# Kernel optimization log

Measured on AMD Instinct MI355X. Metric: run time of the kernel, lower is better.

## Reference

```python
import jax, jax.numpy as jnp
import numpy as np

# model config (see init_kwargs)
L, H, NH, KVH, DH, I, P, F, T = 8, 1024, 16, 2, 64, 4096, 4, 64, 10
QLEN = 9                      # 1 dit token + P cond tokens + P latent tokens
GROUPS = NH // KVH            # GQA repeat factor
PREFIX = P + 1                # prefix_plus
SCALE = DH ** -0.25           # folded into rope cos/sin (applied to q AND k)


def setup_inputs() -> dict:
    key = jax.random.key(0)
    ks = jax.random.split(key, 16)
    g = lambda i, shape, s=0.02: jax.random.normal(ks[i], shape, jnp.float32) * s
    # sway-sampled timestep schedule -> dt table (matches torch precompute)
    ts = np.linspace(1.0, 0.0, T + 1, dtype=np.float32)
    ts = (ts + 1.0 * (np.cos(np.pi / 2 * ts) - 1.0 + ts))[1:]
    dt_all = jnp.asarray((ts[:-1] - ts[1:]).reshape(1, 1, T - 1))
    # rope tables with attention scale folded in
    pos = np.arange(QLEN, dtype=np.float32)
    inv_freq = 1.0 / (10000.0 ** (np.arange(0, DH, 2, dtype=np.float32) / DH))
    freqs = np.concatenate([np.outer(pos, inv_freq)] * 2, axis=-1)  # [QLEN, DH]
    cos_q = jnp.asarray(np.cos(freqs)[None, None] * SCALE)  # [1,1,QLEN,DH]
    sin_q = jnp.asarray(np.sin(freqs)[None, None] * SCALE)
    return dict(
        random=g(0, (1, P, F), 1.0),
        dit_hidden=g(1, (1, 1, H), 1.0),
        feat_cond=g(2, (2, P, H), 1.0),
        cfg_value=jnp.full((1,), 2.5, jnp.float32),
        cfg_value_minus=jnp.full((1,), -1.5, jnp.float32),
        t_all=g(3, (1, T - 1, H), 1.0),   # precomputed time_mlp output table
        dt_all=dt_all, cos_q=cos_q, sin_q=sin_q,
        W_in=g(4, (F, H)), b_in=jnp.zeros((H,), jnp.float32),
        ln1_w=jnp.ones((L, H), jnp.float32),
        Wq=g(5, (L, H, NH * DH)), Wk=g(6, (L, H, KVH * DH)),
        Wv=g(7, (L, H, KVH * DH)), Wo=g(8, (L, NH * DH, H)),
        ln2_w=jnp.ones((L, H), jnp.float32),
        Wg=g(9, (L, H, I)), Wu=g(10, (L, H, I)), Wd=g(11, (L, I, H)),
        norm_w=jnp.ones((H,), jnp.float32),
        W_out=g(12, (H, F)), b_out=jnp.zeros((F,), jnp.float32),
        step=jnp.zeros((1,), jnp.int32),
    )


def _rms(x, w, eps=1e-6):
    return x * jax.lax.rsqrt(jnp.mean(x * x, axis=-1, keepdims=True) + eps) * w


def _rot_half(x):
    x1, x2 = jnp.split(x, 2, axis=-1)
    return jnp.concatenate([-x2, x1], axis=-1)


def reference(random, dit_hidden, feat_cond, cfg_value, cfg_value_minus,
              t_all, dt_all, cos_q, sin_q, W_in, b_in, ln1_w, Wq, Wk, Wv, Wo,
              ln2_w, Wg, Wu, Wd, norm_w, W_out, b_out, step):
    t = t_all[:, step]                                   # [1,1,H]
    dt = dt_all[..., step]                               # [1,1,1]
    dh = jnp.concatenate([dit_hidden + t, t], axis=0)    # CFG doubling -> [2,1,H]
    x = random @ W_in + b_in                             # [1,P,H]
    h = jnp.concatenate([dh, feat_cond, jnp.concatenate([x, x], axis=0)], axis=1)  # [2,QLEN,H]

    def layer(h, p):
        ln1, wq, wk, wv, wo, ln2, wg, wu, wd = p
        hn = _rms(h, ln1)
        q = (hn @ wq).reshape(2, QLEN, NH, DH).transpose(0, 2, 1, 3)
        k = (hn @ wk).reshape(2, QLEN, KVH, DH).transpose(0, 2, 1, 3)
        v = (hn @ wv).reshape(2, QLEN, KVH, DH).transpose(0, 2, 1, 3)
        # rope with head_dim**-0.25 scale folded into cos/sin (applied to q and k)
        q = q * cos_q + _rot_half(q) * sin_q
        k = k * cos_q + _rot_half(k) * sin_q
        k = jnp.repeat(k, GROUPS, axis=1)                # repeat_k (GQA)
        v = jnp.repeat(v, GROUPS, axis=1)                # repeat_v
        attn = jax.nn.softmax(jnp.einsum('bhqd,bhkd->bhqk', q, k), axis=-1)
        out = jnp.einsum('bhqk,bhkd->bhqd', attn, v)
        out = out.transpose(0, 2, 1, 3).reshape(2, QLEN, NH * DH)
        h = h + out @ wo
        hn2 = _rms(h, ln2)
        h = h + (jax.nn.silu(hn2 @ wg) * (hn2 @ wu)) @ wd
        return h, None

    h, _ = jax.lax.scan(layer, h, (ln1_w, Wq, Wk, Wv, Wo, ln2_w, Wg, Wu, Wd))
    h = _rms(h[:, PREFIX:], norm_w)                      # drop prefix -> [2,P,H]
    out = h @ W_out + b_out                              # [2,P,F]
    pos, neg = out[0:1], out[1:2]
    pf = pos.reshape(1, 1, -1)                           # [1,1,P*F]
    nf = neg.reshape(1, -1, 1)                           # [1,P*F,1]
    st = (pf @ nf) / (jnp.swapaxes(nf, 1, 2) @ nf + 1e-7)  # rescaled CFG, [1,1,1]
    dphi = cfg_value_minus * neg * st + cfg_value * pos
    next_random = random - dt * dphi
    return step + 1, next_random
```

## Files before the change

### kernel.cpp

```cpp
#include <hip/hip_runtime.h>

#define TOKENS 18
#define QLEN 9
#define HDIM 1024
#define IDIM 4096
#define NLAYER 8

#define H_OFF     0u
#define QKV_OFF   18432u
#define QKVP_OFF  41472u
#define OPP_OFF   2990592u
#define WDP_OFF   7709184u
#define GUP_OFF   12427776u
#define OUTP_OFF  17146368u
#define TOTAL_F   17162752u

__device__ __forceinline__ void load8(float4* buf, const float* wp, int cc, int stride) {
#pragma unroll
  for (int j = 0; j < 8; j++)
    buf[j] = *reinterpret_cast<const float4*>(wp + (size_t)(cc * 8 + j) * stride);
}
__device__ __forceinline__ void fma8(float4* acc, const float4* buf,
                                     const float (*sb)[TOKENS], int cc) {
#pragma unroll
  for (int j = 0; j < 8; j++) {
#pragma unroll
    for (int t = 0; t < TOKENS; t++) {
      float bv = sb[cc * 8 + j][t];
      acc[t].x += bv * buf[j].x; acc[t].y += bv * buf[j].y;
      acc[t].z += bv * buf[j].z; acc[t].w += bv * buf[j].w;
    }
  }
}

__device__ __forceinline__ void block_rstd18(const float* __restrict__ h,
                                             float* s_rstd, float* s_red) {
  int tid = threadIdx.x;
  float ss[TOKENS];
#pragma unroll
  for (int t = 0; t < TOKENS; t++) {
    float4 v = reinterpret_cast<const float4*>(h + (size_t)t * HDIM)[tid];
    ss[t] = v.x*v.x + v.y*v.y + v.z*v.z + v.w*v.w;
  }
#pragma unroll
  for (int off = 32; off >= 1; off >>= 1) {
#pragma unroll
    for (int t = 0; t < TOKENS; t++) ss[t] += __shfl_down(ss[t], off);
  }
  int wave = tid >> 6, lane = tid & 63;
  if (lane == 0) {
#pragma unroll
    for (int t = 0; t < TOKENS; t++) s_red[wave * TOKENS + t] = ss[t];
  }
  __syncthreads();
  if (tid < TOKENS) {
    float tot = s_red[tid] + s_red[TOKENS + tid] + s_red[2*TOKENS + tid] + s_red[3*TOKENS + tid];
    s_rstd[tid] = rsqrtf(tot * (1.0f / HDIM) + 1e-6f);
  }
  __syncthreads();
}

__global__ __launch_bounds__(256) void k_red4(
    const float* __restrict__ src, float* __restrict__ dst,
    int nparts, int n, int accum) {
  int le = threadIdx.x & 63, j = threadIdx.x >> 6;
  int e = blockIdx.x * 64 + le;
  float s = 0.f;
#pragma unroll 8
  for (int p = j; p < nparts; p += 4) s += src[(size_t)p * n + e];
  __shared__ float red[4][64];
  red[j][le] = s;
  __syncthreads();
  if (j == 0) {
    float tot = red[0][le] + red[1][le] + red[2][le] + red[3][le];
    dst[e] = accum ? dst[e] + tot : tot;
  }
}

__global__ __launch_bounds__(256) void k_embed(
    const float* __restrict__ rnd, const float* __restrict__ dit,
    const float* __restrict__ feat, const float* __restrict__ t_all,
    const float* __restrict__ W_in, const float* __restrict__ b_in,
    const int* __restrict__ step, float* __restrict__ ws) {
  float* h = ws;
  int bid = blockIdx.x, tid = threadIdx.x;
  int st = step[0];
  const float* t = t_all + (size_t)st * HDIM;
  if (bid < 2) {
    int b = bid;
    for (int c = tid; c < HDIM; c += 256) {
      float v = t[c];
      if (b == 0) v += dit[c];
      h[(size_t)(b * QLEN) * HDIM + c] = v;
    }
  } else if (bid < 10) {
    int i = bid - 2;
    int b = i >> 2, p = i & 3;
    for (int c = tid; c < HDIM; c += 256)
      h[(size_t)(b * QLEN + 1 + p) * HDIM + c] = feat[(size_t)(b * 4 + p) * HDIM + c];
  } else {
    int p = bid - 10;
    __shared__ float rl[64];
    if (tid < 64) rl[tid] = rnd[p * 64 + tid];
    __syncthreads();
    for (int c = tid; c < HDIM; c += 256) {
      float acc = b_in[c];
#pragma unroll 8
      for (int f = 0; f < 64; f++) acc += rl[f] * W_in[(size_t)f * HDIM + c];
      h[(size_t)(5 + p) * HDIM + c] = acc;
      h[(size_t)(QLEN + 5 + p) * HDIM + c] = acc;
    }
  }
}

__global__ __launch_bounds__(256) void k_qkv(
    const float* __restrict__ Wq, const float* __restrict__ Wk,
    const float* __restrict__ Wv, const float* __restrict__ ln1,
    float* __restrict__ ws, int layer) {
  const float* h = ws;
  __shared__ float s_rstd[TOKENS];
  __shared__ float s_red[4 * TOKENS];
  __shared__ float s_b[8][TOKENS];
  int tid = threadIdx.x;
  block_rstd18(h, s_rstd, s_red);
  int r0 = blockIdx.y * 8;
  const float* lw = ln1 + (size_t)layer * HDIM;
  for (int i = tid; i < 8 * TOKENS; i += 256) {
    int r = i / TOKENS, t = i - r * TOKENS;
    s_b[r][t] = h[(size_t)t * HDIM + r0 + r] * lw[r0 + r];
  }
  __syncthreads();
  float* qpb = ws + QKVP_OFF + (size_t)blockIdx.y * (TOKENS * 1280);
  if (blockIdx.x == 0) {
    int c = tid * 4;
    const float* wp = Wq + ((size_t)layer << 20) + (size_t)r0 * HDIM + c;
    float4 A[8];
    load8(A, wp, 0, HDIM);
    float4 acc[TOKENS];
#pragma unroll
    for (int t = 0; t < TOKENS; t++) acc[t] = make_float4(0.f, 0.f, 0.f, 0.f);
    fma8(acc, A, s_b, 0);
#pragma unroll
    for (int t = 0; t < TOKENS; t++) {
      float rs = s_rstd[t];
      float4 o = make_float4(acc[t].x*rs, acc[t].y*rs, acc[t].z*rs, acc[t].w*rs);
      *reinterpret_cast<float4*>(qpb + (size_t)t * 1280 + c) = o;
    }
  } else if (tid < 64) {
    int c = 1024 + tid * 4;
    const float* wp;
    if (c < 1152) wp = Wk + (size_t)layer * 131072 + (size_t)r0 * 128 + (c - 1024);
    else          wp = Wv + (size_t)layer * 131072 + (size_t)r0 * 128 + (c - 1152);
    float4 A[8];
    load8(A, wp, 0, 128);
    float4 acc[TOKENS];
#pragma unroll
    for (int t = 0; t < TOKENS; t++) acc[t] = make_float4(0.f, 0.f, 0.f, 0.f);
    fma8(acc, A, s_b, 0);
#pragma unroll
    for (int t = 0; t < TOKENS; t++) {
      float rs = s_rstd[t];
      float4 o = make_float4(acc[t].x*rs, acc[t].y*rs, acc[t].z*rs, acc[t].w*rs);
      *reinterpret_cast<float4*>(qpb + (size_t)t * 1280 + c) = o;
    }
  }
}

__global__ __launch_bounds__(256) void k_attn(
    const float* __restrict__ Wo, const float* __restrict__ cosq,
    const float* __restrict__ sinq, float* __restrict__ ws, int layer) {
  const float* qkv = ws + QKV_OFF;
  int by = blockIdx.x;
  float* op = ws + OPP_OFF + (size_t)by * (TOKENS * HDIM);
  __shared__ float lq[2][QLEN][68];
  __shared__ float lk[2][QLEN][68];
  __shared__ float lv[2][QLEN][4];
  __shared__ float sP[2][QLEN][12];
  __shared__ float sA[4][TOKENS];
  int tid = threadIdx.x;
  int r0 = by * 4;
  int head = r0 >> 6;
  int kvh = head >> 3;
  int d0 = r0 & 63;
  for (int i = tid; i < 2 * QLEN * 64; i += 256) {
    int d = i & 63;
    int qi = (i >> 6) % QLEN;
    int b = i / (QLEN * 64);
    const float* qr = qkv + (size_t)(b * QLEN + qi) * 1280;
    float c = cosq[qi * 64 + d], s = sinq[qi * 64 + d];
    float qv = qr[head * 64 + d];
    float qo = (d < 32) ? -qr[head * 64 + d + 32] : qr[head * 64 + d - 32];
    lq[b][qi][d] = qv * c + qo * s;
    float kv = qr[1024 + kvh * 64 + d];
    float ko = (d < 32) ? -qr[1024 + kvh * 64 + d + 32] : qr[1024 + kvh * 64 + d - 32];
    lk[b][qi][d] = kv * c + ko * s;
  }
  for (int i = tid; i < 2 * QLEN * 4; i += 256) {
    int d = i & 3;
    int ki = (i >> 2) % QLEN;
    int b = i / (QLEN * 4);
    lv[b][ki][d] = qkv[(size_t)(b * QLEN + ki) * 1280 + 1152 + kvh * 64 + d0 + d];
  }
  __syncthreads();
  for (int i = tid; i < 2 * QLEN * QLEN; i += 256) {
    int ki = i % QLEN;
    int qi = (i / QLEN) % QLEN;
    int b = i / (QLEN * QLEN);
    float s = 0.f;
#pragma unroll
    for (int d = 0; d < 64; d++) s += lq[b][qi][d] * lk[b][ki][d];
    sP[b][qi][ki] = s;
  }
  __syncthreads();
  if (tid < TOKENS) {
    int b = tid / QLEN, qi = tid % QLEN;
    float m = -1e30f;
#pragma unroll
    for (int k = 0; k < QLEN; k++) m = fmaxf(m, sP[b][qi][k]);
    float e[QLEN], sum = 0.f;
#pragma unroll
    for (int k = 0; k < QLEN; k++) { e[k] = expf(sP[b][qi][k] - m); sum += e[k]; }
    float inv = 1.f / sum;
#pragma unroll
    for (int k = 0; k < QLEN; k++) sP[b][qi][k] = e[k] * inv;
  }
  __syncthreads();
  for (int i = tid; i < 4 * TOKENS; i += 256) {
    int dd = i / TOKENS, t = i - dd * TOKENS;
    int b = t / QLEN, qi = t % QLEN;
    float a = 0.f;
#pragma unroll
    for (int k = 0; k < QLEN; k++) a += sP[b][qi][k] * lv[b][k][dd];
    sA[dd][t] = a;
  }
  __syncthreads();
  int c = tid * 4;
  const float* wp = Wo + ((size_t)layer << 20) + (size_t)r0 * HDIM + c;
  float4 wv[4];
#pragma unroll
  for (int r = 0; r < 4; r++)
    wv[r] = *reinterpret_cast<const float4*>(wp + (size_t)r * HDIM);
  float4 acc[TOKENS];
#pragma unroll
  for (int t = 0; t < TOKENS; t++) acc[t] = make_float4(0.f, 0.f, 0.f, 0.f);
#pragma unroll
  for (int r = 0; r < 4; r++) {
#pragma unroll
    for (int t = 0; t < TOKENS; t++) {
      float bv = sA[r][t];
      acc[t].x += bv * wv[r].x; acc[t].y += bv * wv[r].y;
      acc[t].z += bv * wv[r].z; acc[t].w += bv * wv[r].w;
    }
  }
#pragma unroll
  for (int t = 0; t < TOKENS; t++)
    *reinterpret_cast<float4*>(op + (size_t)t * HDIM + c) = acc[t];
}

__global__ __launch_bounds__(256) void k_gu(
    const float* __restrict__ Wg, const float* __restrict__ Wu,
    const float* __restrict__ ln2, float* __restrict__ ws, int layer) {
  const float* h = ws;
  __shared__ float s_rstd[TOKENS];
  __shared__ float s_red[4 * TOKENS];
  __shared__ float s_b[32][TOKENS];
  int tid = threadIdx.x;
  block_rstd18(h, s_rstd, s_red);
  int cg = blockIdx.x, ks = blockIdx.y, r0 = ks * 32;
  const float* lw = ln2 + (size_t)layer * HDIM;
  for (int i = tid; i < 32 * TOKENS; i += 256) {
    int r = i / TOKENS, t = i - r * TOKENS;
    s_b[r][t] = h[(size_t)t * HDIM + r0 + r] * lw[r0 + r];
  }
  __syncthreads();
  const float* W = (cg < 4 ? Wg : Wu) + ((size_t)layer << 22);
  int c = (cg & 3) * 1024 + tid * 4;
  const float* wp = W + (size_t)r0 * IDIM + c;
  float4 A[8], B[8];
  float4 acc[TOKENS];
#pragma unroll
  for (int t = 0; t < TOKENS; t++) acc[t] = make_float4(0.f, 0.f, 0.f, 0.f);
  load8(A, wp, 0, IDIM);
  load8(B, wp, 1, IDIM);
  fma8(acc, A, s_b, 0);
  load8(A, wp, 2, IDIM);
  fma8(acc, B, s_b, 1);
  load8(B, wp, 3, IDIM);
  fma8(acc, A, s_b, 2);
  fma8(acc, B, s_b, 3);
  float* gp = ws + GUP_OFF + (size_t)ks * (TOKENS * 8192) + cg * 1024 + tid * 4;
#pragma unroll
  for (int t = 0; t < TOKENS; t++) {
    float rs = s_rstd[t];
    float4 o = make_float4(acc[t].x*rs, acc[t].y*rs, acc[t].z*rs, acc[t].w*rs);
    *reinterpret_cast<float4*>(gp + (size_t)t * 8192) = o;
  }
}

__global__ __launch_bounds__(256) void k_wd(
    const float* __restrict__ Wd, float* __restrict__ ws, int layer) {
  const float* gup = ws + GUP_OFF;
  int by = blockIdx.x;
  int r0 = by * 16;
  __shared__ float s_b[16][TOKENS];
  int tid = threadIdx.x;
  for (int i = tid; i < 16 * TOKENS; i += 256) {
    int r = i / TOKENS, t = i - r * TOKENS;
    const float* base = gup + (size_t)t * 8192 + r0 + r;
    float g = 0.f, u = 0.f;
#pragma unroll 8
    for (int p = 0; p < 32; p++) {
      g += base[(size_t)p * (TOKENS * 8192)];
      u += base[(size_t)p * (TOKENS * 8192) + 4096];
    }
    s_b[r][t] = (g / (1.f + expf(-g))) * u;
  }
  __syncthreads();
  int c = tid * 4;
  const float* wp = Wd + ((size_t)layer << 22) + (size_t)r0 * HDIM + c;
  float4 A[8], B[8];
  float4 acc[TOKENS];
#pragma unroll
  for (int t = 0; t < TOKENS; t++) acc[t] = make_float4(0.f, 0.f, 0.f, 0.f);
  load8(A, wp, 0, HDIM);
  load8(B, wp, 1, HDIM);
  fma8(acc, A, s_b, 0);
  fma8(acc, B, s_b, 1);
  float* wdp = ws + WDP_OFF + (size_t)by * (TOKENS * HDIM);
#pragma unroll
  for (int t = 0; t < TOKENS; t++)
    *reinterpret_cast<float4*>(wdp + (size_t)t * HDIM + c) = acc[t];
}

__global__ __launch_bounds__(256) void k_out(
    const float* __restrict__ Wout, const float* __restrict__ normw,
    float* __restrict__ ws) {
  const float* h = ws;
  float* outp = ws + OUTP_OFF;
  __shared__ float s_rstd[8];
  __shared__ float s_red[32];
  __shared__ float s_b[128][8];
  int tid = threadIdx.x;
  float ss[8];
#pragma unroll
  for (int s = 0; s < 8; s++) {
    int tix = (s >> 2) * QLEN + 5 + (s & 3);
    float4 v = reinterpret_cast<const float4*>(h + (size_t)tix * HDIM)[tid];
    ss[s] = v.x*v.x + v.y*v.y + v.z*v.z + v.w*v.w;
  }
#pragma unroll
  for (int off = 32; off >= 1; off >>= 1) {
#pragma unroll
    for (int s = 0; s < 8; s++) ss[s] += __shfl_down(ss[s], off);
  }
  int wave = tid >> 6, lane = tid & 63;
  if (lane == 0) {
#pragma unroll
    for (int s = 0; s < 8; s++) s_red[wave * 8 + s] = ss[s];
  }
  __syncthreads();
  if (tid < 8) {
    float tot = s_red[tid] + s_red[8 + tid] + s_red[16 + tid] + s_red[24 + tid];
    s_rstd[tid] = rsqrtf(tot * (1.f / HDIM) + 1e-6f);
  }
  __syncthreads();
  int r0 = blockIdx.x * 128;
  for (int i = tid; i < 128 * 8; i += 256) {
    int r = i >> 3, s = i & 7;
    int tix = (s >> 2) * QLEN + 5 + (s & 3);
    s_b[r][s] = h[(size_t)tix * HDIM + r0 + r] * normw[r0 + r] * s_rstd[s];
  }
  __syncthreads();
  int colc = tid & 63, rsub = tid >> 6;
  const float* wp = Wout + (size_t)(r0 + rsub * 32) * 64 + colc;
  float acc[8];
#pragma unroll
  for (int s = 0; s < 8; s++) acc[s] = 0.f;
#pragma unroll 8
  for (int r = 0; r < 32; r++) {
    float w = wp[(size_t)r * 64];
#pragma unroll
    for (int s = 0; s < 8; s++) acc[s] += s_b[rsub * 32 + r][s] * w;
  }
  float* slot = outp + (size_t)(blockIdx.x * 4 + rsub) * 512;
#pragma unroll
  for (int s = 0; s < 8; s++) slot[s * 64 + colc] = acc[s];
}

__global__ __launch_bounds__(256) void k_final(
    const float* __restrict__ rnd, const float* __restrict__ cfg,
    const float* __restrict__ cfgm, const float* __restrict__ dt_all,
    const float* __restrict__ bout, const int* __restrict__ step,
    const float* __restrict__ ws, float* __restrict__ out) {
  const float* outp = ws + OUTP_OFF;
  int tid = threadIdx.x;
  int f = tid & 63;
  float p = bout[f], n = bout[f];
#pragma unroll 8
  for (int pp = 0; pp < 32; pp++) {
    p += outp[(size_t)pp * 512 + tid];
    n += outp[(size_t)pp * 512 + 256 + tid];
  }
  float pn = p * n, nn = n * n;
#pragma unroll
  for (int off = 32; off >= 1; off >>= 1) {
    pn += __shfl_down(pn, off);
    nn += __shfl_down(nn, off);
  }
  __shared__ float red[8];
  __shared__ float s_st;
  int wave = tid >> 6, lane = tid & 63;
  if (lane == 0) { red[wave] = pn; red[4 + wave] = nn; }
  __syncthreads();
  if (tid == 0) {
    float PN = red[0] + red[1] + red[2] + red[3];
    float NN = red[4] + red[5] + red[6] + red[7];
    s_st = PN / (NN + 1e-7f);
  }
  __syncthreads();
  int st = step[0];
  float dphi = cfgm[0] * n * s_st + cfg[0] * p;
  float next = rnd[tid] - dt_all[st] * dphi;
  if (tid == 0) out[0] = (float)(st + 1);
  out[1 + tid] = next;
}

extern "C" void kernel_launch(void* const* d_in, const int* in_sizes, int n_in,
                              void* d_out, int out_size, void* d_ws, size_t ws_size,
                              hipStream_t stream) {
  const float* rnd   = (const float*)d_in[0];
  const float* dit   = (const float*)d_in[1];
  const float* feat  = (const float*)d_in[2];
  const float* cfg   = (const float*)d_in[3];
  const float* cfgm  = (const float*)d_in[4];
  const float* t_all = (const float*)d_in[5];
  const float* dt_al = (const float*)d_in[6];
  const float* cosq  = (const float*)d_in[7];
  const float* sinq  = (const float*)d_in[8];
  const float* W_in  = (const float*)d_in[9];
  const float* b_in  = (const float*)d_in[10];
  const float* ln1   = (const float*)d_in[11];
  const float* Wq    = (const float*)d_in[12];
  const float* Wk    = (const float*)d_in[13];
  const float* Wv    = (const float*)d_in[14];
  const float* Wo    = (const float*)d_in[15];
  const float* ln2   = (const float*)d_in[16];
  const float* Wg    = (const float*)d_in[17];
  const float* Wu    = (const float*)d_in[18];
  const float* Wd    = (const float*)d_in[19];
  const float* normw = (const float*)d_in[20];
  const float* Wout  = (const float*)d_in[21];
  const float* bout  = (const float*)d_in[22];
  const int*   step  = (const int*)d_in[23];
  float* ws = (float*)d_ws;

  k_embed<<<14, 256, 0, stream>>>(rnd, dit, feat, t_all, W_in, b_in, step, ws);
  for (int l = 0; l < NLAYER; l++) {
    k_qkv<<<dim3(2, 128), 256, 0, stream>>>(Wq, Wk, Wv, ln1, ws, l);
    k_red4<<<360, 256, 0, stream>>>(ws + QKVP_OFF, ws + QKV_OFF, 128, TOKENS * 1280, 0);
    k_attn<<<256, 256, 0, stream>>>(Wo, cosq, sinq, ws, l);
    k_red4<<<288, 256, 0, stream>>>(ws + OPP_OFF, ws + H_OFF, 256, TOKENS * HDIM, 1);
    k_gu<<<dim3(8, 32), 256, 0, stream>>>(Wg, Wu, ln2, ws, l);
    k_wd<<<256, 256, 0, stream>>>(Wd, ws, l);
    k_red4<<<288, 256, 0, stream>>>(ws + WDP_OFF, ws + H_OFF, 256, TOKENS * HDIM, 1);
  }
  k_out<<<8, 256, 0, stream>>>(Wout, normw, ws);
  k_final<<<1, 256, 0, stream>>>(rnd, cfg, cfgm, dt_al, bout, step, ws, (float*)d_out);
}
```

Baseline: 620.6 us.

## Fuse split-K reductions and RMS statistics into neighboring layer kernels

Removes the standalone partial-sum reduction kernels. The attention-output and MLP-down reductions are folded into the gate/up and residual-update kernels, and the residual stream is double-buffered. Per-token sum-of-squares partials are produced wherever the hidden state is written, so each matmul kernel no longer recomputes the RMS norm over the full hidden state. The split-K partitioning is retiled for QKV, Wo and gate/up. An atomic counter with a spin-wait is added so one set of blocks can publish the post-attention rstd to the others. This trades fewer launches and less redundant traffic for redundant partial-sum reads in many blocks and a cross-block dependency that could stall if blocks are not co-resident.

```diff
diff --git a/kernel.cpp b/kernel.cpp
--- a/kernel.cpp
+++ b/kernel.cpp
@@ -6,14 +6,18 @@
 #define IDIM 4096
 #define NLAYER 8
 
-#define H_OFF     0u
-#define QKV_OFF   18432u
-#define QKVP_OFF  41472u
-#define OPP_OFF   2990592u
-#define WDP_OFF   7709184u
-#define GUP_OFF   12427776u
-#define OUTP_OFF  17146368u
-#define TOTAL_F   17162752u
+#define HA_OFF    0u
+#define HB_OFF    18432u
+#define SQP_OFF   36864u
+#define RSTD_OFF  37008u
+#define CNT_OFF   37152u
+#define QKVR_OFF  37248u
+#define QKVP_OFF  60288u
+#define OPP_OFF   797568u
+#define GUP_OFF   1387392u
+#define WDP_OFF   10824576u
+#define OUTP_OFF  15543168u
+#define TOTAL_F   15559552u
 
 __device__ __forceinline__ void load8(float4* buf, const float* wp, int cc, int stride) {
 #pragma unroll
@@ -32,48 +36,32 @@
     }
   }
 }
-
-__device__ __forceinline__ void block_rstd18(const float* __restrict__ h,
-                                             float* s_rstd, float* s_red) {
-  int tid = threadIdx.x;
-  float ss[TOKENS];
-#pragma unroll
-  for (int t = 0; t < TOKENS; t++) {
-    float4 v = reinterpret_cast<const float4*>(h + (size_t)t * HDIM)[tid];
-    ss[t] = v.x*v.x + v.y*v.y + v.z*v.z + v.w*v.w;
-  }
-#pragma unroll
-  for (int off = 32; off >= 1; off >>= 1) {
-#pragma unroll
-    for (int t = 0; t < TOKENS; t++) ss[t] += __shfl_down(ss[t], off);
-  }
-  int wave = tid >> 6, lane = tid & 63;
-  if (lane == 0) {
-#pragma unroll
-    for (int t = 0; t < TOKENS; t++) s_red[wave * TOKENS + t] = ss[t];
-  }
-  __syncthreads();
-  if (tid < TOKENS) {
-    float tot = s_red[tid] + s_red[TOKENS + tid] + s_red[2*TOKENS + tid] + s_red[3*TOKENS + tid];
-    s_rstd[tid] = rsqrtf(tot * (1.0f / HDIM) + 1e-6f);
-  }
-  __syncthreads();
-}
-
-__global__ __launch_bounds__(256) void k_red4(
-    const float* __restrict__ src, float* __restrict__ dst,
-    int nparts, int n, int accum) {
-  int le = threadIdx.x & 63, j = threadIdx.x >> 6;
-  int e = blockIdx.x * 64 + le;
-  float s = 0.f;
-#pragma unroll 8
-  for (int p = j; p < nparts; p += 4) s += src[(size_t)p * n + e];
-  __shared__ float red[4][64];
-  red[j][le] = s;
-  __syncthreads();
-  if (j == 0) {
-    float tot = red[0][le] + red[1][le] + red[2][le] + red[3][le];
-    dst[e] = accum ? dst[e] + tot : tot;
+__device__ __forceinline__ void loadf2(float2* buf, const float* wp, int base, int stride) {
+#pragma unroll
+  for (int j = 0; j < 8; j++)
+    buf[j] = *reinterpret_cast<const float2*>(wp + (size_t)(base + j) * stride);
+}
+__device__ __forceinline__ void fmaf2(float2* acc, const float2* buf,
+                                      const float (*sb)[TOKENS], int base) {
+#pragma unroll
+  for (int j = 0; j < 8; j++) {
+#pragma unroll
+    for (int t = 0; t < TOKENS; t++) {
+      float bv = sb[base + j][t];
+      acc[t].x += bv * buf[j].x; acc[t].y += bv * buf[j].y;
+    }
+  }
+}
+__device__ __forceinline__ void loadf1(float* buf, const float* wp, int base, int stride) {
+#pragma unroll
+  for (int j = 0; j < 8; j++) buf[j] = wp[(size_t)(base + j) * stride];
+}
+__device__ __forceinline__ void fmaf1(float* acc, const float* buf,
+                                      const float (*sb)[TOKENS], int base) {
+#pragma unroll
+  for (int j = 0; j < 8; j++) {
+#pragma unroll
+    for (int t = 0; t < TOKENS; t++) acc[t] += sb[base + j][t] * buf[j];
   }
 }
 
@@ -82,110 +70,118 @@
     const float* __restrict__ feat, const float* __restrict__ t_all,
     const float* __restrict__ W_in, const float* __restrict__ b_in,
     const int* __restrict__ step, float* __restrict__ ws) {
-  float* h = ws;
-  int bid = blockIdx.x, tid = threadIdx.x;
+  int t = blockIdx.x >> 3, ch = blockIdx.x & 7, c0 = ch * 128;
+  int b = t / QLEN, q = t - b * QLEN;
+  int tid = threadIdx.x;
+  __shared__ float hv[128];
+  __shared__ float red[2][128];
+  __shared__ float pr[2];
   int st = step[0];
-  const float* t = t_all + (size_t)st * HDIM;
-  if (bid < 2) {
-    int b = bid;
-    for (int c = tid; c < HDIM; c += 256) {
-      float v = t[c];
-      if (b == 0) v += dit[c];
-      h[(size_t)(b * QLEN) * HDIM + c] = v;
-    }
-  } else if (bid < 10) {
-    int i = bid - 2;
-    int b = i >> 2, p = i & 3;
-    for (int c = tid; c < HDIM; c += 256)
-      h[(size_t)(b * QLEN + 1 + p) * HDIM + c] = feat[(size_t)(b * 4 + p) * HDIM + c];
+  if (q < 5) {
+    if (tid < 128) {
+      int c = c0 + tid;
+      float v;
+      if (q == 0) v = t_all[(size_t)st * HDIM + c] + (b == 0 ? dit[c] : 0.f);
+      else        v = feat[(size_t)(b * 4 + q - 1) * HDIM + c];
+      hv[tid] = v;
+    }
   } else {
-    int p = bid - 10;
-    __shared__ float rl[64];
-    if (tid < 64) rl[tid] = rnd[p * 64 + tid];
+    int p = q - 5;
+    int el = tid & 127, hf = tid >> 7;
+    float a = 0.f;
+#pragma unroll
+    for (int f = 0; f < 32; f++) a += rnd[p * 64 + hf * 32 + f] * W_in[(size_t)(hf * 32 + f) * HDIM + c0 + el];
+    red[hf][el] = a;
     __syncthreads();
-    for (int c = tid; c < HDIM; c += 256) {
-      float acc = b_in[c];
-#pragma unroll 8
-      for (int f = 0; f < 64; f++) acc += rl[f] * W_in[(size_t)f * HDIM + c];
-      h[(size_t)(5 + p) * HDIM + c] = acc;
-      h[(size_t)(QLEN + 5 + p) * HDIM + c] = acc;
-    }
-  }
+    if (tid < 128) hv[tid] = red[0][tid] + red[1][tid] + b_in[c0 + tid];
+  }
+  __syncthreads();
+  if (tid < 128) ws[HA_OFF + (size_t)t * HDIM + c0 + tid] = hv[tid];
+  if (tid < 64) {
+    float s = hv[tid] * hv[tid] + hv[tid + 64] * hv[tid + 64];
+#pragma unroll
+    for (int off = 32; off >= 1; off >>= 1) s += __shfl_down(s, off);
+    if (tid == 0) pr[0] = s;
+  }
+  __syncthreads();
+  if (tid == 0) ws[SQP_OFF + (size_t)t * 8 + ch] = pr[0];
 }
 
 __global__ __launch_bounds__(256) void k_qkv(
     const float* __restrict__ Wq, const float* __restrict__ Wk,
     const float* __restrict__ Wv, const float* __restrict__ ln1,
     float* __restrict__ ws, int layer) {
-  const float* h = ws;
+  int ks = blockIdx.y, r0 = ks * 32, bx = blockIdx.x, tid = threadIdx.x;
+  __shared__ float s_b[32][TOKENS];
   __shared__ float s_rstd[TOKENS];
-  __shared__ float s_red[4 * TOKENS];
-  __shared__ float s_b[8][TOKENS];
-  int tid = threadIdx.x;
-  block_rstd18(h, s_rstd, s_red);
-  int r0 = blockIdx.y * 8;
+  if (tid < TOKENS) {
+    float s = 0.f;
+#pragma unroll
+    for (int ch = 0; ch < 8; ch++) s += ws[SQP_OFF + (size_t)tid * 8 + ch];
+    s_rstd[tid] = rsqrtf(s * (1.f / HDIM) + 1e-6f);
+  }
   const float* lw = ln1 + (size_t)layer * HDIM;
-  for (int i = tid; i < 8 * TOKENS; i += 256) {
-    int r = i / TOKENS, t = i - r * TOKENS;
-    s_b[r][t] = h[(size_t)t * HDIM + r0 + r] * lw[r0 + r];
-  }
-  __syncthreads();
-  float* qpb = ws + QKVP_OFF + (size_t)blockIdx.y * (TOKENS * 1280);
-  if (blockIdx.x == 0) {
-    int c = tid * 4;
-    const float* wp = Wq + ((size_t)layer << 20) + (size_t)r0 * HDIM + c;
-    float4 A[8];
-    load8(A, wp, 0, HDIM);
-    float4 acc[TOKENS];
-#pragma unroll
-    for (int t = 0; t < TOKENS; t++) acc[t] = make_float4(0.f, 0.f, 0.f, 0.f);
-    fma8(acc, A, s_b, 0);
+  for (int i = tid; i < 576; i += 256) {
+    int t = i >> 5, r = i & 31;
+    s_b[r][t] = ws[HA_OFF + (size_t)t * HDIM + r0 + r] * lw[r0 + r];
+  }
+  __syncthreads();
+  float* qp = ws + QKVP_OFF + (size_t)ks * (TOKENS * 1280);
+  if (bx < 2) {
+    int col = bx * 512 + tid * 2;
+    const float* wp = Wq + ((size_t)layer << 20) + (size_t)r0 * HDIM + col;
+    float2 A[8], B[8];
+    float2 acc[TOKENS];
+#pragma unroll
+    for (int t = 0; t < TOKENS; t++) acc[t] = make_float2(0.f, 0.f);
+    loadf2(A, wp, 0, HDIM); loadf2(B, wp, 8, HDIM);
+    fmaf2(acc, A, s_b, 0);  loadf2(A, wp, 16, HDIM);
+    fmaf2(acc, B, s_b, 8);  loadf2(B, wp, 24, HDIM);
+    fmaf2(acc, A, s_b, 16); fmaf2(acc, B, s_b, 24);
 #pragma unroll
     for (int t = 0; t < TOKENS; t++) {
       float rs = s_rstd[t];
-      float4 o = make_float4(acc[t].x*rs, acc[t].y*rs, acc[t].z*rs, acc[t].w*rs);
-      *reinterpret_cast<float4*>(qpb + (size_t)t * 1280 + c) = o;
-    }
-  } else if (tid < 64) {
-    int c = 1024 + tid * 4;
-    const float* wp;
-    if (c < 1152) wp = Wk + (size_t)layer * 131072 + (size_t)r0 * 128 + (c - 1024);
-    else          wp = Wv + (size_t)layer * 131072 + (size_t)r0 * 128 + (c - 1152);
-    float4 A[8];
-    load8(A, wp, 0, 128);
-    float4 acc[TOKENS];
-#pragma unroll
-    for (int t = 0; t < TOKENS; t++) acc[t] = make_float4(0.f, 0.f, 0.f, 0.f);
-    fma8(acc, A, s_b, 0);
-#pragma unroll
-    for (int t = 0; t < TOKENS; t++) {
-      float rs = s_rstd[t];
-      float4 o = make_float4(acc[t].x*rs, acc[t].y*rs, acc[t].z*rs, acc[t].w*rs);
-      *reinterpret_cast<float4*>(qpb + (size_t)t * 1280 + c) = o;
-    }
-  }
-}
-
-__global__ __launch_bounds__(256) void k_attn(
+      *reinterpret_cast<float2*>(qp + (size_t)t * 1280 + col) = make_float2(acc[t].x * rs, acc[t].y * rs);
+    }
+  } else {
+    int c = tid;
+    const float* wp = (c < 128)
+      ? (Wk + (size_t)layer * 131072 + (size_t)r0 * 128 + c)
+      : (Wv + (size_t)layer * 131072 + (size_t)r0 * 128 + (c - 128));
+    float A[8], B[8];
+    float acc[TOKENS];
+#pragma unroll
+    for (int t = 0; t < TOKENS; t++) acc[t] = 0.f;
+    loadf1(A, wp, 0, 128); loadf1(B, wp, 8, 128);
+    fmaf1(acc, A, s_b, 0);  loadf1(A, wp, 16, 128);
+    fmaf1(acc, B, s_b, 8);  loadf1(B, wp, 24, 128);
+    fmaf1(acc, A, s_b, 16); fmaf1(acc, B, s_b, 24);
+#pragma unroll
+    for (int t = 0; t < TOKENS; t++) qp[(size_t)t * 1280 + 1024 + c] = acc[t] * s_rstd[t];
+  }
+}
+
+__global__ __launch_bounds__(256) void k_redq(float* __restrict__ ws) {
+  int el = blockIdx.x * 256 + threadIdx.x;
+  float s = 0.f;
+#pragma unroll 8
+  for (int p = 0; p < 32; p++) s += ws[QKVP_OFF + (size_t)p * (TOKENS * 1280) + el];
+  ws[QKVR_OFF + el] = s;
+}
+
+__global__ __launch_bounds__(256) void k_wo(
     const float* __restrict__ Wo, const float* __restrict__ cosq,
     const float* __restrict__ sinq, float* __restrict__ ws, int layer) {
-  const float* qkv = ws + QKV_OFF;
-  int by = blockIdx.x;
-  float* op = ws + OPP_OFF + (size_t)by * (TOKENS * HDIM);
+  const float* qkv = ws + QKVR_OFF;
+  int bx = blockIdx.x, by = blockIdx.y, tid = threadIdx.x;
+  int r0 = by * 32, head = r0 >> 6, kvh = head >> 3, d0 = r0 & 63;
   __shared__ float lq[2][QLEN][68];
   __shared__ float lk[2][QLEN][68];
-  __shared__ float lv[2][QLEN][4];
+  __shared__ float lv[2][QLEN][33];
   __shared__ float sP[2][QLEN][12];
-  __shared__ float sA[4][TOKENS];
-  int tid = threadIdx.x;
-  int r0 = by * 4;
-  int head = r0 >> 6;
-  int kvh = head >> 3;
-  int d0 = r0 & 63;
+  __shared__ float sA[32][TOKENS];
   for (int i = tid; i < 2 * QLEN * 64; i += 256) {
-    int d = i & 63;
-    int qi = (i >> 6) % QLEN;
-    int b = i / (QLEN * 64);
+    int d = i & 63, qi = (i >> 6) % QLEN, b = i / (QLEN * 64);
     const float* qr = qkv + (size_t)(b * QLEN + qi) * 1280;
     float c = cosq[qi * 64 + d], s = sinq[qi * 64 + d];
     float qv = qr[head * 64 + d];
@@ -195,17 +191,13 @@
     float ko = (d < 32) ? -qr[1024 + kvh * 64 + d + 32] : qr[1024 + kvh * 64 + d - 32];
     lk[b][qi][d] = kv * c + ko * s;
   }
-  for (int i = tid; i < 2 * QLEN * 4; i += 256) {
-    int d = i & 3;
-    int ki = (i >> 2) % QLEN;
-    int b = i / (QLEN * 4);
+  for (int i = tid; i < 2 * QLEN * 32; i += 256) {
+    int d = i & 31, ki = (i >> 5) % QLEN, b = i / (QLEN * 32);
     lv[b][ki][d] = qkv[(size_t)(b * QLEN + ki) * 1280 + 1152 + kvh * 64 + d0 + d];
   }
   __syncthreads();
   for (int i = tid; i < 2 * QLEN * QLEN; i += 256) {
-    int ki = i % QLEN;
-    int qi = (i / QLEN) % QLEN;
-    int b = i / (QLEN * QLEN);
+    int ki = i % QLEN, qi = (i / QLEN) % QLEN, b = i / (QLEN * QLEN);
     float s = 0.f;
 #pragma unroll
     for (int d = 0; d < 64; d++) s += lq[b][qi][d] * lk[b][ki][d];
@@ -225,7 +217,7 @@
     for (int k = 0; k < QLEN; k++) sP[b][qi][k] = e[k] * inv;
   }
   __syncthreads();
-  for (int i = tid; i < 4 * TOKENS; i += 256) {
+  for (int i = tid; i < 32 * TOKENS; i += 256) {
     int dd = i / TOKENS, t = i - dd * TOKENS;
     int b = t / QLEN, qi = t % QLEN;
     float a = 0.f;
@@ -234,43 +226,61 @@
     sA[dd][t] = a;
   }
   __syncthreads();
-  int c = tid * 4;
-  const float* wp = Wo + ((size_t)layer << 20) + (size_t)r0 * HDIM + c;
-  float4 wv[4];
-#pragma unroll
-  for (int r = 0; r < 4; r++)
-    wv[r] = *reinterpret_cast<const float4*>(wp + (size_t)r * HDIM);
-  float4 acc[TOKENS];
-#pragma unroll
-  for (int t = 0; t < TOKENS; t++) acc[t] = make_float4(0.f, 0.f, 0.f, 0.f);
-#pragma unroll
-  for (int r = 0; r < 4; r++) {
-#pragma unroll
-    for (int t = 0; t < TOKENS; t++) {
-      float bv = sA[r][t];
-      acc[t].x += bv * wv[r].x; acc[t].y += bv * wv[r].y;
-      acc[t].z += bv * wv[r].z; acc[t].w += bv * wv[r].w;
-    }
-  }
+  int col = bx * 512 + tid * 2;
+  const float* wp = Wo + ((size_t)layer << 20) + (size_t)r0 * HDIM + col;
+  float2 A[8], B[8];
+  float2 acc[TOKENS];
+#pragma unroll
+  for (int t = 0; t < TOKENS; t++) acc[t] = make_float2(0.f, 0.f);
+  loadf2(A, wp, 0, HDIM); loadf2(B, wp, 8, HDIM);
+  fmaf2(acc, A, sA, 0);   loadf2(A, wp, 16, HDIM);
+  fmaf2(acc, B, sA, 8);   loadf2(B, wp, 24, HDIM);
+  fmaf2(acc, A, sA, 16);  fmaf2(acc, B, sA, 24);
+  float* op = ws + OPP_OFF + (size_t)by * (TOKENS * HDIM);
 #pragma unroll
   for (int t = 0; t < TOKENS; t++)
-    *reinterpret_cast<float4*>(op + (size_t)t * HDIM + c) = acc[t];
+    *reinterpret_cast<float2*>(op + (size_t)t * HDIM + col) = acc[t];
 }
 
 __global__ __launch_bounds__(256) void k_gu(
     const float* __restrict__ Wg, const float* __restrict__ Wu,
     const float* __restrict__ ln2, float* __restrict__ ws, int layer) {
-  const float* h = ws;
+  int cg = blockIdx.x, ksx = blockIdx.y, r0 = ksx * 16, tid = threadIdx.x;
+  unsigned* cnt = (unsigned*)(ws + CNT_OFF) + layer;
+  float* rstd_ws = ws + RSTD_OFF + (size_t)layer * TOKENS;
+  __shared__ float s_b[16][TOKENS];
   __shared__ float s_rstd[TOKENS];
-  __shared__ float s_red[4 * TOKENS];
-  __shared__ float s_b[32][TOKENS];
-  int tid = threadIdx.x;
-  block_rstd18(h, s_rstd, s_red);
-  int cg = blockIdx.x, ks = blockIdx.y, r0 = ks * 32;
+  __shared__ float pr[4];
+  if (cg == 0 && ksx < TOKENS) {
+    int t = ksx, c4 = tid * 4;
+    float4 s = *reinterpret_cast<const float4*>(ws + HA_OFF + (size_t)t * HDIM + c4);
+    const float* opp = ws + OPP_OFF + (size_t)t * HDIM + c4;
+#pragma unroll 8
+    for (int p = 0; p < 32; p++) {
+      float4 o = *reinterpret_cast<const float4*>(opp + (size_t)p * (TOKENS * HDIM));
+      s.x += o.x; s.y += o.y; s.z += o.z; s.w += o.w;
+    }
+    *reinterpret_cast<float4*>(ws + HB_OFF + (size_t)t * HDIM + c4) = s;
+    float sq = s.x * s.x + s.y * s.y + s.z * s.z + s.w * s.w;
+#pragma unroll
+    for (int off = 32; off >= 1; off >>= 1) sq += __shfl_down(sq, off);
+    if ((tid & 63) == 0) pr[tid >> 6] = sq;
+    __syncthreads();
+    if (tid == 0) {
+      float tot = pr[0] + pr[1] + pr[2] + pr[3];
+      rstd_ws[t] = rsqrtf(tot * (1.f / HDIM) + 1e-6f);
+      __threadfence();
+      __hip_atomic_fetch_add(cnt, 1u, __ATOMIC_RELEASE, __HIP_MEMORY_SCOPE_AGENT);
+    }
+  }
   const float* lw = ln2 + (size_t)layer * HDIM;
-  for (int i = tid; i < 32 * TOKENS; i += 256) {
-    int r = i / TOKENS, t = i - r * TOKENS;
-    s_b[r][t] = h[(size_t)t * HDIM + r0 + r] * lw[r0 + r];
+  for (int i = tid; i < 288; i += 256) {
+    int t = i >> 4, r = i & 15;
+    const float* pp = ws + OPP_OFF + (size_t)t * HDIM + r0 + r;
+    float v = ws[HA_OFF + (size_t)t * HDIM + r0 + r];
+#pragma unroll 8
+    for (int p = 0; p < 32; p++) v += pp[(size_t)p * (TOKENS * HDIM)];
+    s_b[r][t] = v * lw[r0 + r];
   }
   __syncthreads();
   const float* W = (cg < 4 ? Wg : Wu) + ((size_t)layer << 22);
@@ -283,35 +293,36 @@
   load8(A, wp, 0, IDIM);
   load8(B, wp, 1, IDIM);
   fma8(acc, A, s_b, 0);
-  load8(A, wp, 2, IDIM);
   fma8(acc, B, s_b, 1);
-  load8(B, wp, 3, IDIM);
-  fma8(acc, A, s_b, 2);
-  fma8(acc, B, s_b, 3);
-  float* gp = ws + GUP_OFF + (size_t)ks * (TOKENS * 8192) + cg * 1024 + tid * 4;
+  if (tid == 0) {
+    while (__hip_atomic_load(cnt, __ATOMIC_ACQUIRE, __HIP_MEMORY_SCOPE_AGENT) < (unsigned)TOKENS)
+      __builtin_amdgcn_s_sleep(2);
+  }
+  __syncthreads();
+  if (tid < TOKENS) s_rstd[tid] = rstd_ws[tid];
+  __syncthreads();
+  float* gp = ws + GUP_OFF + (size_t)ksx * (TOKENS * 8192) + cg * 1024 + tid * 4;
 #pragma unroll
   for (int t = 0; t < TOKENS; t++) {
     float rs = s_rstd[t];
-    float4 o = make_float4(acc[t].x*rs, acc[t].y*rs, acc[t].z*rs, acc[t].w*rs);
-    *reinterpret_cast<float4*>(gp + (size_t)t * 8192) = o;
+    *reinterpret_cast<float4*>(gp + (size_t)t * 8192) =
+      make_float4(acc[t].x * rs, acc[t].y * rs, acc[t].z * rs, acc[t].w * rs);
   }
 }
 
 __global__ __launch_bounds__(256) void k_wd(
     const float* __restrict__ Wd, float* __restrict__ ws, int layer) {
-  const float* gup = ws + GUP_OFF;
-  int by = blockIdx.x;
-  int r0 = by * 16;
+  int bid = blockIdx.x, tid = threadIdx.x;
+  int r0 = bid * 16;
   __shared__ float s_b[16][TOKENS];
-  int tid = threadIdx.x;
-  for (int i = tid; i < 16 * TOKENS; i += 256) {
-    int r = i / TOKENS, t = i - r * TOKENS;
-    const float* base = gup + (size_t)t * 8192 + r0 + r;
+  for (int i = tid; i < 288; i += 256) {
+    int t = i >> 4, r = i & 15;
+    const float* gp = ws + GUP_OFF + (size_t)t * 8192 + r0 + r;
     float g = 0.f, u = 0.f;
 #pragma unroll 8
-    for (int p = 0; p < 32; p++) {
-      g += base[(size_t)p * (TOKENS * 8192)];
-      u += base[(size_t)p * (TOKENS * 8192) + 4096];
+    for (int p = 0; p < 64; p++) {
+      g += gp[(size_t)p * (TOKENS * 8192)];
+      u += gp[(size_t)p * (TOKENS * 8192) + 4096];
     }
     s_b[r][t] = (g / (1.f + expf(-g))) * u;
   }
@@ -326,42 +337,51 @@
   load8(B, wp, 1, HDIM);
   fma8(acc, A, s_b, 0);
   fma8(acc, B, s_b, 1);
-  float* wdp = ws + WDP_OFF + (size_t)by * (TOKENS * HDIM);
+  float* wdp = ws + WDP_OFF + (size_t)bid * (TOKENS * HDIM);
 #pragma unroll
   for (int t = 0; t < TOKENS; t++)
     *reinterpret_cast<float4*>(wdp + (size_t)t * HDIM + c) = acc[t];
+}
+
+__global__ __launch_bounds__(256) void k_hup(float* __restrict__ ws) {
+  int t = blockIdx.x >> 3, ch = blockIdx.x & 7, c0 = ch * 128;
+  int tid = threadIdx.x;
+  int el = tid & 127, hf = tid >> 7;
+  __shared__ float red[2][128];
+  __shared__ float pr[2];
+  float s = 0.f;
+  const float* wp = ws + WDP_OFF + (size_t)t * HDIM + c0 + el;
+#pragma unroll 8
+  for (int p = hf * 128; p < hf * 128 + 128; p++) s += wp[(size_t)p * (TOKENS * HDIM)];
+  red[hf][el] = s;
+  __syncthreads();
+  float hn = 0.f;
+  if (tid < 128) {
+    hn = ws[HB_OFF + (size_t)t * HDIM + c0 + tid] + red[0][tid] + red[1][tid];
+    ws[HA_OFF + (size_t)t * HDIM + c0 + tid] = hn;
+    float sq = hn * hn;
+#pragma unroll
+    for (int off = 32; off >= 1; off >>= 1) sq += __shfl_down(sq, off);
+    if ((tid & 63) == 0) pr[tid >> 6] = sq;
+  }
+  __syncthreads();
+  if (tid == 0) ws[SQP_OFF + (size_t)t * 8 + ch] = pr[0] + pr[1];
 }
 
 __global__ __launch_bounds__(256) void k_out(
     const float* __restrict__ Wout, const float* __restrict__ normw,
     float* __restrict__ ws) {
-  const float* h = ws;
+  const float* h = ws + HA_OFF;
   float* outp = ws + OUTP_OFF;
   __shared__ float s_rstd[8];
-  __shared__ float s_red[32];
   __shared__ float s_b[128][8];
   int tid = threadIdx.x;
-  float ss[8];
-#pragma unroll
-  for (int s = 0; s < 8; s++) {
-    int tix = (s >> 2) * QLEN + 5 + (s & 3);
-    float4 v = reinterpret_cast<const float4*>(h + (size_t)tix * HDIM)[tid];
-    ss[s] = v.x*v.x + v.y*v.y + v.z*v.z + v.w*v.w;
-  }
-#pragma unroll
-  for (int off = 32; off >= 1; off >>= 1) {
-#pragma unroll
-    for (int s = 0; s < 8; s++) ss[s] += __shfl_down(ss[s], off);
-  }
-  int wave = tid >> 6, lane = tid & 63;
-  if (lane == 0) {
-#pragma unroll
-    for (int s = 0; s < 8; s++) s_red[wave * 8 + s] = ss[s];
-  }
-  __syncthreads();
   if (tid < 8) {
-    float tot = s_red[tid] + s_red[8 + tid] + s_red[16 + tid] + s_red[24 + tid];
-    s_rstd[tid] = rsqrtf(tot * (1.f / HDIM) + 1e-6f);
+    int tix = (tid >> 2) * QLEN + 5 + (tid & 3);
+    float s = 0.f;
+#pragma unroll
+    for (int ch = 0; ch < 8; ch++) s += ws[SQP_OFF + (size_t)tix * 8 + ch];
+    s_rstd[tid] = rsqrtf(s * (1.f / HDIM) + 1e-6f);
   }
   __syncthreads();
   int r0 = blockIdx.x * 128;
@@ -454,15 +474,16 @@
   const int*   step  = (const int*)d_in[23];
   float* ws = (float*)d_ws;
 
-  k_embed<<<14, 256, 0, stream>>>(rnd, dit, feat, t_all, W_in, b_in, step, ws);
+  hipMemsetAsync((void*)(ws + CNT_OFF), 0, 64 * sizeof(unsigned), stream);
+
+  k_embed<<<144, 256, 0, stream>>>(rnd, dit, feat, t_all, W_in, b_in, step, ws);
   for (int l = 0; l < NLAYER; l++) {
-    k_qkv<<<dim3(2, 128), 256, 0, stream>>>(Wq, Wk, Wv, ln1, ws, l);
-    k_red4<<<360, 256, 0, stream>>>(ws + QKVP_OFF, ws + QKV_OFF, 128, TOKENS * 1280, 0);
-    k_attn<<<256, 256, 0, stream>>>(Wo, cosq, sinq, ws, l);
-    k_red4<<<288, 256, 0, stream>>>(ws + OPP_OFF, ws + H_OFF, 256, TOKENS * HDIM, 1);
-    k_gu<<<dim3(8, 32), 256, 0, stream>>>(Wg, Wu, ln2, ws, l);
+    k_qkv<<<dim3(3, 32), 256, 0, stream>>>(Wq, Wk, Wv, ln1, ws, l);
+    k_redq<<<90, 256, 0, stream>>>(ws);
+    k_wo<<<dim3(2, 32), 256, 0, stream>>>(Wo, cosq, sinq, ws, l);
+    k_gu<<<dim3(8, 64), 256, 0, stream>>>(Wg, Wu, ln2, ws, l);
     k_wd<<<256, 256, 0, stream>>>(Wd, ws, l);
-    k_red4<<<288, 256, 0, stream>>>(ws + WDP_OFF, ws + H_OFF, 256, TOKENS * HDIM, 1);
+    k_hup<<<144, 256, 0, stream>>>(ws);
   }
   k_out<<<8, 256, 0, stream>>>(Wout, normw, ws);
   k_final<<<1, 256, 0, stream>>>(rnd, cfg, cfgm, dt_al, bout, step, ws, (float*)d_out);
```

Result: slower. 840.6 us (+35.5%).
